# Optimization experiments

Measured on AMD Instinct MI355X. Metric: run time of the kernel, lower is better.

The kernel has to match this reference:

```python
import jax, jax.numpy as jnp
import numpy as np

N = 100000   # n_nodes
E = 1000000  # n_edges
B = 2000     # batch of interactions
K = 20       # n_neighbors
D = 172      # memory/node/edge/embedding dim
T = 172      # time encoding dim
MSG = 2 * D + D + T  # 688, identity message function
HEADS = 2


def setup_inputs() -> dict:
    key = jax.random.key(0)
    ks = jax.random.split(key, 32)
    g = lambda i, shape, fan: jax.random.normal(ks[i], shape, jnp.float32) / np.float32(np.sqrt(fan))
    inp = {}
    inp['memory'] = jax.random.normal(ks[0], (N, D), jnp.float32)
    inp['messages'] = jax.random.normal(ks[1], (N, MSG), jnp.float32)
    inp['edge_features'] = jax.random.normal(ks[2], (E, D), jnp.float32)
    inp['edge_times'] = jax.random.uniform(ks[3], (B,), jnp.float32) * 10000.0
    inp['neighbor_times'] = jax.random.uniform(ks[4], (3 * B, K), jnp.float32) * 10000.0
    # TimeEncode init: w = 1 / 10^linspace(0, 9, T)
    inp['time_w'] = jnp.asarray(1.0 / 10.0 ** np.linspace(0, 9, T), jnp.float32)
    inp['time_b'] = jnp.zeros((T,), jnp.float32)
    # GRUCell params
    inp['gru_w_ih'] = g(5, (3 * D, MSG), MSG)
    inp['gru_w_hh'] = g(6, (3 * D, D), D)
    inp['gru_b_ih'] = jnp.zeros((3 * D,), jnp.float32)
    inp['gru_b_hh'] = jnp.zeros((3 * D,), jnp.float32)
    # temporal attention params: query = [feat||time], key = [feat||edge||time]
    inp['w_q'] = g(7, (D, D + T), D + T)
    inp['w_k'] = g(8, (D, D + D + T), D + D + T)
    inp['w_v'] = g(9, (D, D + D + T), D + D + T)
    inp['w_o'] = g(10, (D, D), D)
    # MergeLayer(attn_out, src_feat)
    inp['merge_w1'] = g(11, (D, 2 * D), 2 * D)
    inp['merge_b1'] = jnp.zeros((D,), jnp.float32)
    inp['merge_w2'] = g(12, (D, D), D)
    inp['merge_b2'] = jnp.zeros((D,), jnp.float32)
    # affinity MergeLayer -> scalar score
    inp['aff_w1'] = g(13, (D, 2 * D), 2 * D)
    inp['aff_b1'] = jnp.zeros((D,), jnp.float32)
    inp['aff_w2'] = g(14, (1, D), D)
    inp['aff_b2'] = jnp.zeros((1,), jnp.float32)
    inp['source_nodes'] = jax.random.randint(ks[15], (B,), 0, N, jnp.int32)
    inp['destination_nodes'] = jax.random.randint(ks[16], (B,), 0, N, jnp.int32)
    inp['negative_nodes'] = jax.random.randint(ks[17], (B,), 0, N, jnp.int32)
    inp['neighbors'] = jax.random.randint(ks[18], (3 * B, K), 0, N, jnp.int32)
    inp['neighbor_edge_idxs'] = jax.random.randint(ks[19], (3 * B, K), 0, E, jnp.int32)
    return inp


def reference(memory, messages, edge_features, edge_times, neighbor_times,
              time_w, time_b, gru_w_ih, gru_w_hh, gru_b_ih, gru_b_hh,
              w_q, w_k, w_v, w_o, merge_w1, merge_b1, merge_w2, merge_b2,
              aff_w1, aff_b1, aff_w2, aff_b2,
              source_nodes, destination_nodes, negative_nodes,
              neighbors, neighbor_edge_idxs):
    d = memory.shape[1]
    dh = d // HEADS
    k_nbr = neighbors.shape[1]

    def time_enc(t):  # TimeEncode: cos(t * w + b)
        return jnp.cos(t[..., None] * time_w + time_b)

    # --- GRU memory update from aggregated ('last') messages ---
    gi = messages @ gru_w_ih.T + gru_b_ih          # [N, 3D]
    gh = memory @ gru_w_hh.T + gru_b_hh            # [N, 3D]
    i_r, i_z, i_n = jnp.split(gi, 3, axis=-1)
    h_r, h_z, h_n = jnp.split(gh, 3, axis=-1)
    r = jax.nn.sigmoid(i_r + h_r)
    z = jax.nn.sigmoid(i_z + h_z)
    n = jnp.tanh(i_n + r * h_n)
    mem_upd = (1.0 - z) * n + z * memory           # [N, D]

    # --- temporal graph attention embedding (1 layer) ---
    nodes = jnp.concatenate([source_nodes, destination_nodes, negative_nodes])  # [3B]
    ts = jnp.concatenate([edge_times, edge_times, edge_times])                  # [3B]
    m = nodes.shape[0]
    src_feat = mem_upd[nodes]                                                   # [3B, D]
    q_in = jnp.concatenate([src_feat, time_enc(jnp.zeros_like(ts))], axis=-1)   # [3B, D+T]
    nbr_feat = mem_upd[neighbors]                                               # [3B, K, D]
    e_feat = edge_features[neighbor_edge_idxs]                                  # [3B, K, D]
    dt = ts[:, None] - neighbor_times                                           # [3B, K]
    k_in = jnp.concatenate([nbr_feat, e_feat, time_enc(dt)], axis=-1)           # [3B, K, 2D+T]

    q = (q_in @ w_q.T).reshape(m, HEADS, dh)
    kk = (k_in @ w_k.T).reshape(m, k_nbr, HEADS, dh)
    vv = (k_in @ w_v.T).reshape(m, k_nbr, HEADS, dh)
    scores = jnp.einsum('nhd,nkhd->nhk', q, kk) / np.float32(np.sqrt(dh))
    valid = (neighbors > 0)[:, None, :]            # node 0 is the pad node
    scores = jnp.where(valid, scores, jnp.float32(-1e9))
    attn = jax.nn.softmax(scores, axis=-1)
    ctx = jnp.einsum('nhk,nkhd->nhd', attn, vv).reshape(m, d) @ w_o.T
    h1 = jax.nn.relu(jnp.concatenate([ctx, src_feat], axis=-1) @ merge_w1.T + merge_b1)
    emb = h1 @ merge_w2.T + merge_b2               # [3B, D]

    # --- affinity score on (src,dst) and (src,neg) pairs ---
    b = source_nodes.shape[0]
    s_emb, d_emb, n_emb = emb[:b], emb[b:2 * b], emb[2 * b:]
    s_cat = jnp.concatenate([s_emb, s_emb], axis=0)
    d_cat = jnp.concatenate([d_emb, n_emb], axis=0)
    ah = jax.nn.relu(jnp.concatenate([s_cat, d_cat], axis=-1) @ aff_w1.T + aff_b1)
    prob = jax.nn.sigmoid((ah @ aff_w2.T + aff_b2).squeeze(-1))  # [2B]
    return prob[:b], prob[b:]
```

## Files before the change

### kernel.cpp

```cpp
#include <hip/hip_runtime.h>
#include <math.h>

#define N_NODES 100000
#define BATCH   2000
#define KNBR    20
#define DF      172
#define MSGD    688
#define M3      6000
#define DH      86
#define KIN_D   516

#define KA      864
#define JP      768
#define KREAL   860
#define NTILES_N ((N_NODES + 127) / 128)
#define NWG_GRU (NTILES_N * 6)
#define KSTEPS  (KA / 32)

#define NKV     120000
#define KP_KV   544
#define JKV     384
#define KVS     352
#define NKV_TILES ((NKV + 127) / 128)

typedef __bf16 bf16x8 __attribute__((ext_vector_type(8)));
typedef __bf16 bf16x4 __attribute__((ext_vector_type(4)));
typedef float  f32x4  __attribute__((ext_vector_type(4)));

#define WPB_OFF   0
#define BP4_OFF   331776
#define WKV_OFF   332544
#define MU_OFF    436992
#define UNI_OFF   17636992
#define KV_OFF    UNI_OFF
#define QB_OFF    38756992
#define CAT_OFF   39286400
#define H1_OFF    40345216
#define EMBB_OFF  40922752
#define AH_OFF    41452160
#define MW1O_OFF  41812608
#define WQB_OFF   41842192
#define WM1B_OFF  41875984
#define WM2B_OFF  41909776
#define WAFFB_OFF 41928208
#define BM1P_OFF  41962000
#define BM2P_OFF  41962192
#define BAFFP_OFF 41962384
#define BQ0_OFF   41962576
#define NODES_OFF 41962768

__device__ __forceinline__ float sigmoidf_(float x) { return 1.0f / (1.0f + expf(-x)); }

typedef __attribute__((address_space(1))) const void gvoid;
typedef __attribute__((address_space(3))) void svoid;
__device__ __forceinline__ void gl16(const void* g, void* l) {
    __builtin_amdgcn_global_load_lds((gvoid*)g, (svoid*)l, 16, 0, 0);
}

__global__ __launch_bounds__(256) void prep_kernel(
    const float* __restrict__ w_ih, const float* __restrict__ w_hh,
    const float* __restrict__ b_ih, const float* __restrict__ b_hh,
    __bf16* __restrict__ wpb, float* __restrict__ bp4)
{
    int idx = blockIdx.x * 256 + threadIdx.x;
    if (idx < JP * KA) {
        int j = idx / KA, k = idx - j * KA;
        int d = j >> 2, g = j & 3;
        float v = 0.f;
        if (d < DF) {
            if (g == 0) {
                if (k < MSGD) v = w_ih[d * MSGD + k];
// ... 72 lines not shown
    const float* __restrict__ merge_w1, const float* __restrict__ w_o,
    float* __restrict__ mw1o)
{
    int idx = blockIdx.x * 256 + threadIdx.x;
    if (idx >= DF * DF) return;
    int j = idx / DF, k = idx - j * DF;
    float s = 0.f;
    for (int c = 0; c < DF; ++c)
        s = fmaf(merge_w1[j * 344 + c], w_o[c * DF + k], s);
    mw1o[idx] = s;
}

__global__ __launch_bounds__(256) void prep_tail_kernel(
    const float* __restrict__ w_q, const float* __restrict__ mw1o,
    const float* __restrict__ merge_w1, const float* __restrict__ merge_w2,
    const float* __restrict__ aff_w1,
    const float* __restrict__ merge_b1, const float* __restrict__ merge_b2,
    const float* __restrict__ aff_b1,
    const int* __restrict__ src_nodes, const int* __restrict__ dst_nodes,
    const int* __restrict__ neg_nodes,
    __bf16* __restrict__ wqb, __bf16* __restrict__ wm1b,
    __bf16* __restrict__ wm2b, __bf16* __restrict__ waffb,
    float* __restrict__ bm1p, float* __restrict__ bm2p,
    float* __restrict__ baffp, float* __restrict__ bq0,
    int* __restrict__ nodes_cat)
{
    int idx = blockIdx.x * 256 + threadIdx.x;
    if (idx < 192 * 352) {
        int j = idx / 352, k = idx - j * 352;
        float vq = 0.f, vm = 0.f, va = 0.f;
        if (j < DF) {
            if (k < DF) {
                vq = w_q[j * 344 + k];
                vm = mw1o[j * DF + k];
                va = aff_w1[j * 344 + k];
            } else if (k >= 176 && k < 348) {
                vq = w_q[j * 344 + 172 + (k - 176)];
                vm = merge_w1[j * 344 + 172 + (k - 176)];
                va = aff_w1[j * 344 + 172 + (k - 176)];
            }
        }
        wqb[idx] = (__bf16)vq;
        wm1b[idx] = (__bf16)vm;
        waffb[idx] = (__bf16)va;
    }
    if (idx < 192 * 192) {
        int j = idx / 192, k = idx - j * 192;
        wm2b[idx] = (__bf16)((j < DF && k < DF) ? merge_w2[j * DF + k] : 0.f);
    }
    if (idx < 192) {
        bm1p[idx]  = (idx < DF) ? merge_b1[idx] : 0.f;
        bm2p[idx]  = (idx < DF) ? merge_b2[idx] : 0.f;
        baffp[idx] = (idx < DF) ? aff_b1[idx] : 0.f;
        bq0[idx]   = 0.f;
    }
    if (idx < 6016) {
        int i = min(idx, M3 - 1);
        int node;
        if (i < BATCH)          node = src_nodes[i];
        else if (i < 2 * BATCH) node = dst_nodes[i - BATCH];
        else                    node = neg_nodes[i - 2 * BATCH];
        nodes_cat[idx] = node;
    }
}

__global__ __launch_bounds__(256) void gru_mfma3_kernel(
    const __bf16* __restrict__ xb, const __bf16* __restrict__ wpb,
    const float* __restrict__ bp4, const float* __restrict__ memory,
    float* __restrict__ mem_upd)
{
    __shared__ __align__(16) __bf16 Ws[3][128 * 32];
    __shared__ __align__(16) __bf16 Xs[3][128 * 32];

    const int t    = threadIdx.x;
    const int w    = t >> 6, lane = t & 63;
    const int lo   = lane & 15, hi = lane >> 4;
    const int wm   = w >> 1, wn = w & 1;

    const int orig = blockIdx.x;
    const int q = NWG_GRU >> 3, rr = NWG_GRU & 7;
    const int xcd = orig & 7, oidx = orig >> 3;
    const int wgid = (xcd < rr ? xcd * (q + 1) : rr * (q + 1) + (xcd - rr) * q) + oidx;
    const int m_tile = wgid % 6;
    const int n_tile = wgid / 6;
    const int n0 = n_tile * 128;
    const int j0 = m_tile * 128;

    const int srow  = lane >> 2;
    const int sslot = ((lane & 3) ^ ((lane >> 3) & 3)) * 8;

    f32x4 acc[4][4];
#pragma unroll
    for (int mi = 0; mi < 4; ++mi)
#pragma unroll
        for (int ni = 0; ni < 4; ++ni)
            acc[mi][ni] = (f32x4){0.f, 0.f, 0.f, 0.f};

    const __bf16* wbase = wpb + (size_t)j0 * KA;
    const __bf16* xbase = xb + (size_t)n0 * KA;

#define STAGE(buf, k0)                                                          \
    {                                                                           \
        _Pragma("unroll")                                                       \
        for (int qq = 0; qq < 2; ++qq) {                                        \
            const int lr = w * 32 + qq * 16 + srow;                             \
            gl16(wbase + (size_t)lr * KA + (k0) + sslot,                        \
                 &Ws[buf][(w * 32 + qq * 16) * 32]);                            \
            gl16(xbase + (size_t)lr * KA + (k0) + sslot,                        \
                 &Xs[buf][(w * 32 + qq * 16) * 32]);                            \
        }                                                                       \
    }

    STAGE(0, 0);
    STAGE(1, 32);

    const int fsa = (hi ^ ((lo >> 1) & 3)) * 8;
    for (int ks = 0; ks < KSTEPS; ++ks) {
        if (ks < KSTEPS - 1) {
            asm volatile("s_waitcnt vmcnt(4)" ::: "memory");
        } else {
            asm volatile("s_waitcnt vmcnt(0)" ::: "memory");
        }
        __builtin_amdgcn_s_barrier();
        if (ks + 2 < KSTEPS) STAGE((ks + 2) % 3, (ks + 2) * 32);

        const int bi = ks % 3;
        bf16x8 af[4], bx_[4];
#pragma unroll
        for (int i = 0; i < 4; ++i) {
            af[i]  = *(const bf16x8*)&Ws[bi][(wm * 64 + i * 16 + lo) * 32 + fsa];
            bx_[i] = *(const bf16x8*)&Xs[bi][(wn * 64 + i * 16 + lo) * 32 + fsa];
        }
#pragma unroll
        for (int mi = 0; mi < 4; ++mi)
#pragma unroll
            for (int ni = 0; ni < 4; ++ni)
                acc[mi][ni] = __builtin_amdgcn_mfma_f32_16x16x32_bf16(
                    af[mi], bx_[ni], acc[mi][ni], 0, 0, 0);
    }
#undef STAGE

    const int dbase = m_tile * 32 + wm * 16;
#pragma unroll
    for (int mi = 0; mi < 4; ++mi) {
        const int d = dbase + mi * 4 + hi;
        if (d >= DF) continue;
        const float4 b4 = *(const float4*)&bp4[4 * d];
#pragma unroll
        for (int ni = 0; ni < 4; ++ni) {
            const int n = n0 + wn * 64 + ni * 16 + lo;
            if (n >= N_NODES) continue;
            float sr  = acc[mi][ni][0] + b4.x;
            float sz  = acc[mi][ni][1] + b4.y;
            float gin = acc[mi][ni][2] + b4.z;
            float ghn = acc[mi][ni][3] + b4.w;
            float mem = memory[(size_t)n * DF + d];
            float rg  = sigmoidf_(sr);
            float zg  = sigmoidf_(sz);
            float nt  = tanhf(fmaf(rg, ghn, gin));
            mem_upd[(size_t)n * DF + d] = fmaf(zg, mem - nt, nt);
        }
    }
}

__global__ __launch_bounds__(256) void kv_gemm2_kernel(
    const float* __restrict__ mem_upd, const float* __restrict__ edge_features,
    const float* __restrict__ edge_times, const float* __restrict__ neighbor_times,
    const float* __restrict__ time_w, const float* __restrict__ time_b,
    const int* __restrict__ neighbors, const int* __restrict__ nbr_eidx,
    const __bf16* __restrict__ wkvb, __bf16* __restrict__ kv)
{
    __shared__ __align__(16) __bf16 Ws[128][32];
    __shared__ __align__(16) __bf16 Xs[128][32];

    const int t    = threadIdx.x;
    const int w    = t >> 6, lane = t & 63;
    const int lo   = lane & 15, hi = lane >> 4;
    const int wm   = w >> 1, wn = w & 1;

    const int bx     = blockIdx.x;
    const int n_tile = bx / 3;
    const int m_tile = bx - n_tile * 3;
    const int n0     = n_tile * 128;
    const int j0     = m_tile * 128;

    const int xrow  = t >> 1, xhalf = t & 1;
    const int nr    = min(n0 + xrow, NKV - 1);
    const int nbr   = neighbors[nr];
    const int eidx  = nbr_eidx[nr];
    const float dt  = edge_times[(nr / KNBR) % BATCH] - neighbor_times[nr];
    const float* mrow = mem_upd       + (size_t)nbr  * DF;
    const float* erow = edge_features + (size_t)eidx * DF;
    const __bf16* wrow = wkvb + (size_t)(j0 + xrow) * KP_KV;

    f32x4 acc[4][4];
#pragma unroll
    for (int mi = 0; mi < 4; ++mi)
#pragma unroll
        for (int ni = 0; ni < 4; ++ni)
            acc[mi][ni] = (f32x4){0.f, 0.f, 0.f, 0.f};

#define LOADX(k0, dst)                                                          \
    {                                                                           \
        _Pragma("unroll")                                                       \
        for (int c = 0; c < 4; ++c) {                                           \
            const int kb = (k0) + xhalf * 16 + c * 4;                           \
            float4 v;                                                           \
            if (kb < DF) {                                                      \
                v = *(const float4*)(mrow + kb);                                \
            } else if (kb < 2 * DF) {                                           \
                v = *(const float4*)(erow + (kb - DF));                         \
            } else if (kb < KIN_D) {                                            \
                const float4 tw = *(const float4*)(time_w + (kb - 2 * DF));     \
                const float4 tb = *(const float4*)(time_b + (kb - 2 * DF));     \
                v.x = cosf(fmaf(dt, tw.x, tb.x));                               \
                v.y = cosf(fmaf(dt, tw.y, tb.y));                               \
                v.z = cosf(fmaf(dt, tw.z, tb.z));                               \
                v.w = cosf(fmaf(dt, tw.w, tb.w));                               \
            } else {                                                            \
                v = make_float4(0.f, 0.f, 0.f, 0.f);                            \
            }                                                                   \
            dst[c] = v;                                                         \
        }                                                                       \
    }

    float4 xf[4];
    bf16x8 wp0, wp1;
    LOADX(0, xf);
    wp0 = *(const bf16x8*)(wrow + xhalf * 16);
    wp1 = *(const bf16x8*)(wrow + xhalf * 16 + 8);

    for (int ks = 0; ks < KP_KV / 32; ++ks) {
        const int k0 = ks * 32;
        bf16x8 x0, x1;
        x0[0]=(__bf16)xf[0].x; x0[1]=(__bf16)xf[0].y; x0[2]=(__bf16)xf[0].z; x0[3]=(__bf16)xf[0].w;
        x0[4]=(__bf16)xf[1].x; x0[5]=(__bf16)xf[1].y; x0[6]=(__bf16)xf[1].z; x0[7]=(__bf16)xf[1].w;
        x1[0]=(__bf16)xf[2].x; x1[1]=(__bf16)xf[2].y; x1[2]=(__bf16)xf[2].z; x1[3]=(__bf16)xf[2].w;
        x1[4]=(__bf16)xf[3].x; x1[5]=(__bf16)xf[3].y; x1[6]=(__bf16)xf[3].z; x1[7]=(__bf16)xf[3].w;
        *(bf16x8*)&Ws[xrow][xhalf * 16]     = wp0;
        *(bf16x8*)&Ws[xrow][xhalf * 16 + 8] = wp1;
        *(bf16x8*)&Xs[xrow][xhalf * 16]     = x0;
        *(bf16x8*)&Xs[xrow][xhalf * 16 + 8] = x1;

        if (ks + 1 < KP_KV / 32) {
            LOADX(k0 + 32, xf);
            wp0 = *(const bf16x8*)(wrow + k0 + 32 + xhalf * 16);
            wp1 = *(const bf16x8*)(wrow + k0 + 32 + xhalf * 16 + 8);
        }

        asm volatile("s_waitcnt lgkmcnt(0)" ::: "memory");
        __builtin_amdgcn_s_barrier();

        bf16x8 af[4], bx_[4];
#pragma unroll
        for (int i = 0; i < 4; ++i) {
            af[i]  = *(const bf16x8*)&Ws[wm * 64 + i * 16 + lo][hi * 8];
            bx_[i] = *(const bf16x8*)&Xs[wn * 64 + i * 16 + lo][hi * 8];
        }
#pragma unroll
        for (int mi = 0; mi < 4; ++mi)
#pragma unroll
            for (int ni = 0; ni < 4; ++ni)
                acc[mi][ni] = __builtin_amdgcn_mfma_f32_16x16x32_bf16(
                    af[mi], bx_[ni], acc[mi][ni], 0, 0, 0);

        __builtin_amdgcn_s_barrier();
    }
#undef LOADX

#pragma unroll
    for (int mi = 0; mi < 4; ++mi) {
        const int jb = j0 + wm * 64 + mi * 16 + hi * 4;
        int off;
        if (jb + 3 < DF)                 off = jb;
        else if (jb >= 192 && jb < 361)  off = jb - 16;
        else continue;
#pragma unroll
        for (int ni = 0; ni < 4; ++ni) {
            const int n = n0 + wn * 64 + ni * 16 + lo;
            if (n >= NKV) continue;
            bf16x4 o;
            o[0] = (__bf16)acc[mi][ni][0];
            o[1] = (__bf16)acc[mi][ni][1];
            o[2] = (__bf16)acc[mi][ni][2];
            o[3] = (__bf16)acc[mi][ni][3];
            *(bf16x4*)(kv + (size_t)n * KVS + off) = o;
        }
    }
}

template<int MODE, int KP>
__global__ __launch_bounds__(256) void tail_gemm_kernel(
    const __bf16* __restrict__ wb, const float* __restrict__ bias,
    const void* __restrict__ actsrc, const float* __restrict__ time_b,
    const int* __restrict__ nodes_cat,
    __bf16* __restrict__ outb, int ostride, int jmax, int nrows, int relu)
{
    __shared__ __align__(16) __bf16 Ws[128][32];
    __shared__ __align__(16) __bf16 Xs[128][32];

    const int t    = threadIdx.x;
    const int w    = t >> 6, lane = t & 63;
    const int lo   = lane & 15, hi = lane >> 4;
    const int wm   = w >> 1, wn = w & 1;

    const int n_tile = blockIdx.x >> 1;
    const int j0     = (blockIdx.x & 1) * 64;
    const int n0     = n_tile * 128;

    const int xrow  = t >> 1, xhalf = t & 1;
    const int nr    = min(n0 + xrow, nrows - 1);
    const __bf16* wrow = wb + (size_t)(j0 + xrow) * KP;

    f32x4 acc[4][4];
#pragma unroll
    for (int mi = 0; mi < 4; ++mi)
#pragma unroll
        for (int ni = 0; ni < 4; ++ni)
            acc[mi][ni] = (f32x4){0.f, 0.f, 0.f, 0.f};

    for (int k0 = 0; k0 < KP; k0 += 32) {
        bf16x8 w0 = *(const bf16x8*)(wrow + k0 + xhalf * 16);
        bf16x8 w1 = *(const bf16x8*)(wrow + k0 + xhalf * 16 + 8);
        bf16x8 x0, x1;
        const int kb16 = k0 + xhalf * 16;
        if constexpr (MODE == 0) {
            const float* mrow = (const float*)actsrc + (size_t)nodes_cat[nr] * DF;
            float fl[16];
#pragma unroll
            for (int c = 0; c < 4; ++c) {
                const int b = kb16 + c * 4;
                float4 v;
                if (b + 3 < DF) v = *(const float4*)(mrow + b);
                else if (b >= 176 && b < 348) {
                    const float4 tb = *(const float4*)(time_b + (b - 176));
                    v.x = cosf(tb.x); v.y = cosf(tb.y);
                    v.z = cosf(tb.z); v.w = cosf(tb.w);
                } else v = make_float4(0.f, 0.f, 0.f, 0.f);
                fl[c*4+0]=v.x; fl[c*4+1]=v.y; fl[c*4+2]=v.z; fl[c*4+3]=v.w;
            }
#pragma unroll
            for (int jj = 0; jj < 8; ++jj) { x0[jj]=(__bf16)fl[jj]; x1[jj]=(__bf16)fl[8+jj]; }
        } else if constexpr (MODE == 1) {
            const __bf16* arow = (const __bf16*)actsrc + (size_t)nr * KP;
            x0 = *(const bf16x8*)(arow + kb16);
            x1 = *(const bf16x8*)(arow + kb16 + 8);
        } else {
            const int s = (nr < BATCH) ? nr : nr - BATCH;
            const __bf16* eb = (const __bf16*)actsrc;
            const __bf16* src = (kb16 < 176) ? (eb + (size_t)s * 176 + kb16)
                                             : (eb + (size_t)(nr + BATCH) * 176 + (kb16 - 176));
            x0 = *(const bf16x8*)src;
            x1 = *(const bf16x8*)(src + 8);
        }
        *(bf16x8*)&Ws[xrow][xhalf * 16]     = w0;
        *(bf16x8*)&Ws[xrow][xhalf * 16 + 8] = w1;
        *(bf16x8*)&Xs[xrow][xhalf * 16]     = x0;
        *(bf16x8*)&Xs[xrow][xhalf * 16 + 8] = x1;
        __syncthreads();

        bf16x8 af[4], bx_[4];
#pragma unroll
        for (int i = 0; i < 4; ++i) {
            af[i]  = *(const bf16x8*)&Ws[wm * 64 + i * 16 + lo][hi * 8];
            bx_[i] = *(const bf16x8*)&Xs[wn * 64 + i * 16 + lo][hi * 8];
        }
#pragma unroll
        for (int mi = 0; mi < 4; ++mi)
#pragma unroll
            for (int ni = 0; ni < 4; ++ni)
                acc[mi][ni] = __builtin_amdgcn_mfma_f32_16x16x32_bf16(
                    af[mi], bx_[ni], acc[mi][ni], 0, 0, 0);
        __syncthreads();
    }

#pragma unroll
    for (int mi = 0; mi < 4; ++mi) {
        const int jb = j0 + wm * 64 + mi * 16 + hi * 4;
        if (jb + 3 >= jmax) continue;
        const float4 b4 = *(const float4*)(bias + jb);
#pragma unroll
        for (int ni = 0; ni < 4; ++ni) {
            const int n = n0 + wn * 64 + ni * 16 + lo;
            if (n >= nrows) continue;
            float v0 = acc[mi][ni][0] + b4.x;
            float v1 = acc[mi][ni][1] + b4.y;
            float v2 = acc[mi][ni][2] + b4.z;
            float v3 = acc[mi][ni][3] + b4.w;
            if (relu) {
                v0 = fmaxf(v0, 0.f); v1 = fmaxf(v1, 0.f);
                v2 = fmaxf(v2, 0.f); v3 = fmaxf(v3, 0.f);
            }
            bf16x4 o;
            o[0]=(__bf16)v0; o[1]=(__bf16)v1; o[2]=(__bf16)v2; o[3]=(__bf16)v3;
            *(bf16x4*)(outb + (size_t)n * ostride + jb) = o;
        }
    }
}

__global__ __launch_bounds__(256) void attn_mid_kernel(
    const float* __restrict__ mem_upd, const __bf16* __restrict__ kv,
    const __bf16* __restrict__ qb, const int* __restrict__ neighbors,
    const int* __restrict__ nodes_cat, __bf16* __restrict__ cat)
{
    __shared__ __align__(16) __bf16 kvs[KNBR][KVS];
    __shared__ float qs[176];
    __shared__ float scl[2][KNBR];
    __shared__ float attnl[2][KNBR];
    __shared__ int   nbrs[KNBR];

    const int i = blockIdx.x;
    const int t = threadIdx.x;

    if (t < KNBR) nbrs[t] = neighbors[i * KNBR + t];
    if (t < 176) qs[t] = (float)qb[(size_t)i * 176 + t];
    {
        const uint4* src = (const uint4*)(kv + (size_t)i * KNBR * KVS);
        uint4* dst = (uint4*)&kvs[0][0];
        for (int idx = t; idx < KNBR * KVS / 8; idx += 256) dst[idx] = src[idx];
    }
    __syncthreads();

    if (t < 2 * KNBR) {
        int h = t / KNBR, kn = t - h * KNBR;
// ... 1 lines not shown
#pragma unroll 2
        for (int j = 0; j < DH; ++j)
            s = fmaf(qs[h * DH + j], (float)kvs[kn][h * DH + j], s);
        s /= sqrtf((float)DH);
        scl[h][kn] = (nbrs[kn] > 0) ? s : -1e9f;
    }
    __syncthreads();
    if (t < 2) {
        float m = -INFINITY;
        for (int kn = 0; kn < KNBR; ++kn) m = fmaxf(m, scl[t][kn]);
        float se = 0.f;
        for (int kn = 0; kn < KNBR; ++kn) se += expf(scl[t][kn] - m);
        float inv = 1.f / se;
        for (int kn = 0; kn < KNBR; ++kn) attnl[t][kn] = expf(scl[t][kn] - m) * inv;
    }
    __syncthreads();
    if (t < DF) {
        int h = t / DH;
        float cx = 0.f;
#pragma unroll
        for (int kn = 0; kn < KNBR; ++kn)
            cx = fmaf(attnl[h][kn], (float)kvs[kn][176 + t], cx);
        cat[(size_t)i * 352 + t] = (__bf16)cx;
        cat[(size_t)i * 352 + 176 + t] =
            (__bf16)mem_upd[(size_t)nodes_cat[i] * DF + t];
    }
    if (t < 4) {
        cat[(size_t)i * 352 + 172 + t] = (__bf16)0.f;
        cat[(size_t)i * 352 + 348 + t] = (__bf16)0.f;
    }
}

__global__ __launch_bounds__(256) void aff_fin_kernel(
    const __bf16* __restrict__ ah, const float* __restrict__ aff_w2,
    const float* __restrict__ aff_b2, float* __restrict__ out)
{
    const int t = threadIdx.x;
    const int w = t >> 6, lane = t & 63;
    const int row = blockIdx.x * 4 + w;
    if (row >= 2 * BATCH) return;
    float s = 0.f;
    if (lane < DF)       s += (float)ah[(size_t)row * 176 + lane] * aff_w2[lane];
    if (lane + 64 < DF)  s += (float)ah[(size_t)row * 176 + lane + 64] * aff_w2[lane + 64];
    if (lane + 128 < DF) s += (float)ah[(size_t)row * 176 + lane + 128] * aff_w2[lane + 128];
#pragma unroll
    for (int off = 32; off > 0; off >>= 1) s += __shfl_down(s, off, 64);
    if (lane == 0) out[row] = 1.f / (1.f + expf(-(s + aff_b2[0])));
}

extern "C" void kernel_launch(void* const* d_in, const int* in_sizes, int n_in,
                              void* d_out, int out_size, void* d_ws, size_t ws_size,
                              hipStream_t stream)
{
    (void)in_sizes; (void)n_in; (void)out_size; (void)ws_size;
    const float* memory         = (const float*)d_in[0];
    const float* messages       = (const float*)d_in[1];
    const float* edge_features  = (const float*)d_in[2];
    const float* edge_times     = (const float*)d_in[3];
    const float* neighbor_times = (const float*)d_in[4];
    const float* time_w         = (const float*)d_in[5];
    const float* time_b         = (const float*)d_in[6];
    const float* gru_w_ih       = (const float*)d_in[7];
    const float* gru_w_hh       = (const float*)d_in[8];
    const float* gru_b_ih       = (const float*)d_in[9];
    const float* gru_b_hh       = (const float*)d_in[10];
    const float* w_q            = (const float*)d_in[11];
    const float* w_k            = (const float*)d_in[12];
    const float* w_v            = (const float*)d_in[13];
    const float* w_o            = (const float*)d_in[14];
    const float* merge_w1       = (const float*)d_in[15];
    const float* merge_b1       = (const float*)d_in[16];
    const float* merge_w2       = (const float*)d_in[17];
    const float* merge_b2       = (const float*)d_in[18];
    const float* aff_w1         = (const float*)d_in[19];
    const float* aff_b1         = (const float*)d_in[20];
    const float* aff_w2         = (const float*)d_in[21];
    const float* aff_b2         = (const float*)d_in[22];
    const int* src_nodes        = (const int*)d_in[23];
    const int* dst_nodes        = (const int*)d_in[24];
    const int* neg_nodes        = (const int*)d_in[25];
    const int* neighbors        = (const int*)d_in[26];
    const int* nbr_eidx         = (const int*)d_in[27];

    float* ws       = (float*)d_ws;
    __bf16* wpb     = (__bf16*)(ws + WPB_OFF);
    float* bp4      = ws + BP4_OFF;
    __bf16* wkvb    = (__bf16*)(ws + WKV_OFF);
    float* mem_upd  = ws + MU_OFF;
    __bf16* xbuf    = (__bf16*)(ws + UNI_OFF);
    __bf16* kv      = (__bf16*)(ws + KV_OFF);
    __bf16* qbuf    = (__bf16*)(ws + QB_OFF);
    __bf16* cat     = (__bf16*)(ws + CAT_OFF);
    __bf16* h1      = (__bf16*)(ws + H1_OFF);
    __bf16* embb    = (__bf16*)(ws + EMBB_OFF);
    __bf16* ah      = (__bf16*)(ws + AH_OFF);
    float* mw1o     = ws + MW1O_OFF;
    __bf16* wqb     = (__bf16*)(ws + WQB_OFF);
    __bf16* wm1b    = (__bf16*)(ws + WM1B_OFF);
    __bf16* wm2b    = (__bf16*)(ws + WM2B_OFF);
    __bf16* waffb   = (__bf16*)(ws + WAFFB_OFF);
    float* bm1p     = ws + BM1P_OFF;
    float* bm2p     = ws + BM2P_OFF;
    float* baffp    = ws + BAFFP_OFF;
    float* bq0      = ws + BQ0_OFF;
    int*   nodes_cat= (int*)(ws + NODES_OFF);
    float* out      = (float*)d_out;

    prep_kernel<<<(JP * KA + 255) / 256, 256, 0, stream>>>(
        gru_w_ih, gru_w_hh, gru_b_ih, gru_b_hh, wpb, bp4);
    prep_kv_kernel<<<(JKV * KP_KV + 255) / 256, 256, 0, stream>>>(w_k, w_v, wkvb);
    conv_kernel<<<2048, 256, 0, stream>>>(messages, memory, xbuf);
    gru_mfma3_kernel<<<NWG_GRU, 256, 0, stream>>>(xbuf, wpb, bp4, memory, mem_upd);
    mw1o_kernel<<<(DF * DF + 255) / 256, 256, 0, stream>>>(merge_w1, w_o, mw1o);
    prep_tail_kernel<<<(192 * 352 + 255) / 256, 256, 0, stream>>>(
        w_q, mw1o, merge_w1, merge_w2, aff_w1, merge_b1, merge_b2, aff_b1,
        src_nodes, dst_nodes, neg_nodes,
        wqb, wm1b, wm2b, waffb, bm1p, bm2p, baffp, bq0, nodes_cat);
    kv_gemm2_kernel<<<NKV_TILES * 3, 256, 0, stream>>>(
        mem_upd, edge_features, edge_times, neighbor_times, time_w, time_b,
        neighbors, nbr_eidx, wkvb, kv);
    tail_gemm_kernel<0, 352><<<47 * 2, 256, 0, stream>>>(
        wqb, bq0, mem_upd, time_b, nodes_cat, qbuf, 176, 176, M3, 0);
    attn_mid_kernel<<<M3, 256, 0, stream>>>(
        mem_upd, kv, qbuf, neighbors, nodes_cat, cat);
    tail_gemm_kernel<1, 352><<<47 * 2, 256, 0, stream>>>(
        wm1b, bm1p, cat, nullptr, nullptr, h1, 192, 192, M3, 1);
    tail_gemm_kernel<1, 192><<<47 * 2, 256, 0, stream>>>(
        wm2b, bm2p, h1, nullptr, nullptr, embb, 176, 176, M3, 0);
    tail_gemm_kernel<2, 352><<<32 * 2, 256, 0, stream>>>(
        waffb, baffp, embb, nullptr, nullptr, ah, 176, 176, 2 * BATCH, 1);
    aff_fin_kernel<<<(2 * BATCH + 3) / 4, 256, 0, stream>>>(ah, aff_w2, aff_b2, out);
}
```

Measured before the change: 763.5 us.

## Widen GRU tiles, store memory in bf16, fuse merge and affinity tail GEMMs

The GRU GEMM now computes 128x256 tiles per workgroup, doubling the node dimension, so each staged weight tile is reused over more nodes. The updated memory is stored as bf16 rather than fp32, which halves its write traffic and the gather reads in the KV, Q and attention kernels. The two merge-layer GEMMs become one kernel with h1 kept in shared memory, and the affinity GEMM is fused with the final dot-product and sigmoid, dropping several launches and intermediate buffers. The risks are extra rounding on memory values and higher register and LDS use in the wider GRU kernel, which may lower occupancy.

```diff
diff --git a/kernel.cpp b/kernel.cpp
--- a/kernel.cpp
+++ b/kernel.cpp
@@ -13,9 +13,9 @@
 #define KA      864
 #define JP      768
 #define KREAL   860
-#define NTILES_N ((N_NODES + 127) / 128)
-#define NWG_GRU (NTILES_N * 6)
 #define KSTEPS  (KA / 32)
+#define NTILES4 391
+#define NWG4    (NTILES4 * 6)
 
 #define NKV     120000
 #define KP_KV   544
@@ -35,9 +35,7 @@
 #define KV_OFF    UNI_OFF
 #define QB_OFF    38756992
 #define CAT_OFF   39286400
-#define H1_OFF    40345216
 #define EMBB_OFF  40922752
-#define AH_OFF    41452160
 #define MW1O_OFF  41812608
 #define WQB_OFF   41842192
 #define WM1B_OFF  41875984
@@ -46,7 +44,6 @@
 #define BM1P_OFF  41962000
 #define BM2P_OFF  41962192
 #define BAFFP_OFF 41962384
-#define BQ0_OFF   41962576
 #define NODES_OFF 41962768
 
 __device__ __forceinline__ float sigmoidf_(float x) { return 1.0f / (1.0f + expf(-x)); }
@@ -165,8 +162,7 @@
     __bf16* __restrict__ wqb, __bf16* __restrict__ wm1b,
     __bf16* __restrict__ wm2b, __bf16* __restrict__ waffb,
     float* __restrict__ bm1p, float* __restrict__ bm2p,
-    float* __restrict__ baffp, float* __restrict__ bq0,
-    int* __restrict__ nodes_cat)
+    float* __restrict__ baffp, int* __restrict__ nodes_cat)
 {
     int idx = blockIdx.x * 256 + threadIdx.x;
     if (idx < 192 * 352) {
@@ -195,7 +191,6 @@
         bm1p[idx]  = (idx < DF) ? merge_b1[idx] : 0.f;
         bm2p[idx]  = (idx < DF) ? merge_b2[idx] : 0.f;
         baffp[idx] = (idx < DF) ? aff_b1[idx] : 0.f;
-        bq0[idx]   = 0.f;
     }
     if (idx < 6016) {
         int i = min(idx, M3 - 1);
@@ -207,13 +202,13 @@
     }
 }
 
-__global__ __launch_bounds__(256) void gru_mfma3_kernel(
+__global__ __launch_bounds__(256) void gru_mfma4_kernel(
     const __bf16* __restrict__ xb, const __bf16* __restrict__ wpb,
     const float* __restrict__ bp4, const float* __restrict__ memory,
-    float* __restrict__ mem_upd)
+    __bf16* __restrict__ mem_upd)
 {
     __shared__ __align__(16) __bf16 Ws[3][128 * 32];
-    __shared__ __align__(16) __bf16 Xs[3][128 * 32];
+    __shared__ __align__(16) __bf16 Xs[3][256 * 32];
 
     const int t    = threadIdx.x;
     const int w    = t >> 6, lane = t & 63;
@@ -221,22 +216,22 @@
     const int wm   = w >> 1, wn = w & 1;
 
     const int orig = blockIdx.x;
-    const int q = NWG_GRU >> 3, rr = NWG_GRU & 7;
+    const int q = NWG4 >> 3, rr = NWG4 & 7;
     const int xcd = orig & 7, oidx = orig >> 3;
     const int wgid = (xcd < rr ? xcd * (q + 1) : rr * (q + 1) + (xcd - rr) * q) + oidx;
     const int m_tile = wgid % 6;
     const int n_tile = wgid / 6;
-    const int n0 = n_tile * 128;
+    const int n0 = n_tile * 256;
     const int j0 = m_tile * 128;
 
     const int srow  = lane >> 2;
     const int sslot = ((lane & 3) ^ ((lane >> 3) & 3)) * 8;
 
-    f32x4 acc[4][4];
+    f32x4 acc[4][8];
 #pragma unroll
     for (int mi = 0; mi < 4; ++mi)
 #pragma unroll
-        for (int ni = 0; ni < 4; ++ni)
+        for (int ni = 0; ni < 8; ++ni)
             acc[mi][ni] = (f32x4){0.f, 0.f, 0.f, 0.f};
 
     const __bf16* wbase = wpb + (size_t)j0 * KA;
@@ -249,8 +244,12 @@
             const int lr = w * 32 + qq * 16 + srow;                             \
             gl16(wbase + (size_t)lr * KA + (k0) + sslot,                        \
                  &Ws[buf][(w * 32 + qq * 16) * 32]);                            \
+        }                                                                       \
+        _Pragma("unroll")                                                       \
+        for (int qq = 0; qq < 4; ++qq) {                                        \
+            const int lr = w * 64 + qq * 16 + srow;                             \
             gl16(xbase + (size_t)lr * KA + (k0) + sslot,                        \
-                 &Xs[buf][(w * 32 + qq * 16) * 32]);                            \
+                 &Xs[buf][(w * 64 + qq * 16) * 32]);                            \
         }                                                                       \
     }
 
@@ -260,7 +259,7 @@
     const int fsa = (hi ^ ((lo >> 1) & 3)) * 8;
     for (int ks = 0; ks < KSTEPS; ++ks) {
         if (ks < KSTEPS - 1) {
-            asm volatile("s_waitcnt vmcnt(4)" ::: "memory");
+            asm volatile("s_waitcnt vmcnt(6)" ::: "memory");
         } else {
             asm volatile("s_waitcnt vmcnt(0)" ::: "memory");
         }
@@ -268,18 +267,19 @@
         if (ks + 2 < KSTEPS) STAGE((ks + 2) % 3, (ks + 2) * 32);
 
         const int bi = ks % 3;
-        bf16x8 af[4], bx_[4];
-#pragma unroll
-        for (int i = 0; i < 4; ++i) {
+        bf16x8 af[4], bxv[8];
+#pragma unroll
+        for (int i = 0; i < 4; ++i)
             af[i]  = *(const bf16x8*)&Ws[bi][(wm * 64 + i * 16 + lo) * 32 + fsa];
-            bx_[i] = *(const bf16x8*)&Xs[bi][(wn * 64 + i * 16 + lo) * 32 + fsa];
-        }
+#pragma unroll
+        for (int i = 0; i < 8; ++i)
+            bxv[i] = *(const bf16x8*)&Xs[bi][(wn * 128 + i * 16 + lo) * 32 + fsa];
 #pragma unroll
         for (int mi = 0; mi < 4; ++mi)
 #pragma unroll
-            for (int ni = 0; ni < 4; ++ni)
+            for (int ni = 0; ni < 8; ++ni)
                 acc[mi][ni] = __builtin_amdgcn_mfma_f32_16x16x32_bf16(
-                    af[mi], bx_[ni], acc[mi][ni], 0, 0, 0);
+                    af[mi], bxv[ni], acc[mi][ni], 0, 0, 0);
     }
 #undef STAGE
 
@@ -290,8 +290,8 @@
         if (d >= DF) continue;
         const float4 b4 = *(const float4*)&bp4[4 * d];
 #pragma unroll
-        for (int ni = 0; ni < 4; ++ni) {
-            const int n = n0 + wn * 64 + ni * 16 + lo;
+        for (int ni = 0; ni < 8; ++ni) {
+            const int n = n0 + wn * 128 + ni * 16 + lo;
             if (n >= N_NODES) continue;
             float sr  = acc[mi][ni][0] + b4.x;
             float sz  = acc[mi][ni][1] + b4.y;
@@ -301,13 +301,13 @@
             float rg  = sigmoidf_(sr);
             float zg  = sigmoidf_(sz);
             float nt  = tanhf(fmaf(rg, ghn, gin));
-            mem_upd[(size_t)n * DF + d] = fmaf(zg, mem - nt, nt);
-        }
-    }
-}
-
-__global__ __launch_bounds__(256) void kv_gemm2_kernel(
-    const float* __restrict__ mem_upd, const float* __restrict__ edge_features,
+            mem_upd[(size_t)n * DF + d] = (__bf16)fmaf(zg, mem - nt, nt);
+        }
+    }
+}
+
+__global__ __launch_bounds__(256) void kv_gemm3_kernel(
+    const __bf16* __restrict__ mem_upd, const float* __restrict__ edge_features,
     const float* __restrict__ edge_times, const float* __restrict__ neighbor_times,
     const float* __restrict__ time_w, const float* __restrict__ time_b,
     const int* __restrict__ neighbors, const int* __restrict__ nbr_eidx,
@@ -332,8 +332,8 @@
     const int nbr   = neighbors[nr];
     const int eidx  = nbr_eidx[nr];
     const float dt  = edge_times[(nr / KNBR) % BATCH] - neighbor_times[nr];
-    const float* mrow = mem_upd       + (size_t)nbr  * DF;
-    const float* erow = edge_features + (size_t)eidx * DF;
+    const __bf16* mrow = mem_upd       + (size_t)nbr  * DF;
+    const float*  erow = edge_features + (size_t)eidx * DF;
     const __bf16* wrow = wkvb + (size_t)(j0 + xrow) * KP_KV;
 
     f32x4 acc[4][4];
@@ -343,50 +343,60 @@
         for (int ni = 0; ni < 4; ++ni)
             acc[mi][ni] = (f32x4){0.f, 0.f, 0.f, 0.f};
 
-#define LOADX(k0, dst)                                                          \
+#define LOADX(k0, xh, xf)                                                       \
     {                                                                           \
         _Pragma("unroll")                                                       \
         for (int c = 0; c < 4; ++c) {                                           \
             const int kb = (k0) + xhalf * 16 + c * 4;                           \
-            float4 v;                                                           \
             if (kb < DF) {                                                      \
-                v = *(const float4*)(mrow + kb);                                \
+                xh[c] = *(const bf16x4*)(mrow + kb);                            \
             } else if (kb < 2 * DF) {                                           \
-                v = *(const float4*)(erow + (kb - DF));                         \
+                xf[c] = *(const float4*)(erow + (kb - DF));                     \
             } else if (kb < KIN_D) {                                            \
                 const float4 tw = *(const float4*)(time_w + (kb - 2 * DF));     \
                 const float4 tb = *(const float4*)(time_b + (kb - 2 * DF));     \
+                float4 v;                                                       \
                 v.x = cosf(fmaf(dt, tw.x, tb.x));                               \
                 v.y = cosf(fmaf(dt, tw.y, tb.y));                               \
                 v.z = cosf(fmaf(dt, tw.z, tb.z));                               \
                 v.w = cosf(fmaf(dt, tw.w, tb.w));                               \
+                xf[c] = v;                                                      \
             } else {                                                            \
-                v = make_float4(0.f, 0.f, 0.f, 0.f);                            \
+                xf[c] = make_float4(0.f, 0.f, 0.f, 0.f);                        \
             }                                                                   \
-            dst[c] = v;                                                         \
         }                                                                       \
     }
 
+    bf16x4 xh[4];
     float4 xf[4];
     bf16x8 wp0, wp1;
-    LOADX(0, xf);
+    LOADX(0, xh, xf);
     wp0 = *(const bf16x8*)(wrow + xhalf * 16);
     wp1 = *(const bf16x8*)(wrow + xhalf * 16 + 8);
 
     for (int ks = 0; ks < KP_KV / 32; ++ks) {
         const int k0 = ks * 32;
         bf16x8 x0, x1;
-        x0[0]=(__bf16)xf[0].x; x0[1]=(__bf16)xf[0].y; x0[2]=(__bf16)xf[0].z; x0[3]=(__bf16)xf[0].w;
-        x0[4]=(__bf16)xf[1].x; x0[5]=(__bf16)xf[1].y; x0[6]=(__bf16)xf[1].z; x0[7]=(__bf16)xf[1].w;
-        x1[0]=(__bf16)xf[2].x; x1[1]=(__bf16)xf[2].y; x1[2]=(__bf16)xf[2].z; x1[3]=(__bf16)xf[2].w;
-        x1[4]=(__bf16)xf[3].x; x1[5]=(__bf16)xf[3].y; x1[6]=(__bf16)xf[3].z; x1[7]=(__bf16)xf[3].w;
+#pragma unroll
+        for (int c = 0; c < 4; ++c) {
+            const int kb = k0 + xhalf * 16 + c * 4;
+            __bf16 e0, e1, e2, e3;
+            if (kb < DF) {
+                e0 = xh[c][0]; e1 = xh[c][1]; e2 = xh[c][2]; e3 = xh[c][3];
+            } else {
+                e0 = (__bf16)xf[c].x; e1 = (__bf16)xf[c].y;
+                e2 = (__bf16)xf[c].z; e3 = (__bf16)xf[c].w;
+            }
+            if (c < 2) { x0[c*4]=e0; x0[c*4+1]=e1; x0[c*4+2]=e2; x0[c*4+3]=e3; }
+            else { x1[(c-2)*4]=e0; x1[(c-2)*4+1]=e1; x1[(c-2)*4+2]=e2; x1[(c-2)*4+3]=e3; }
+        }
         *(bf16x8*)&Ws[xrow][xhalf * 16]     = wp0;
         *(bf16x8*)&Ws[xrow][xhalf * 16 + 8] = wp1;
         *(bf16x8*)&Xs[xrow][xhalf * 16]     = x0;
         *(bf16x8*)&Xs[xrow][xhalf * 16 + 8] = x1;
 
         if (ks + 1 < KP_KV / 32) {
-            LOADX(k0 + 32, xf);
+            LOADX(k0 + 32, xh, xf);
             wp0 = *(const bf16x8*)(wrow + k0 + 32 + xhalf * 16);
             wp1 = *(const bf16x8*)(wrow + k0 + 32 + xhalf * 16 + 8);
         }
@@ -432,12 +442,10 @@
     }
 }
 
-template<int MODE, int KP>
-__global__ __launch_bounds__(256) void tail_gemm_kernel(
-    const __bf16* __restrict__ wb, const float* __restrict__ bias,
-    const void* __restrict__ actsrc, const float* __restrict__ time_b,
-    const int* __restrict__ nodes_cat,
-    __bf16* __restrict__ outb, int ostride, int jmax, int nrows, int relu)
+__global__ __launch_bounds__(256) void q_gemm_kernel(
+    const __bf16* __restrict__ wqb, const __bf16* __restrict__ mem_upd,
+    const float* __restrict__ time_b, const int* __restrict__ nodes_cat,
+    __bf16* __restrict__ qbuf)
 {
     __shared__ __align__(16) __bf16 Ws[128][32];
     __shared__ __align__(16) __bf16 Xs[128][32];
@@ -452,8 +460,9 @@
     const int n0     = n_tile * 128;
 
     const int xrow  = t >> 1, xhalf = t & 1;
-    const int nr    = min(n0 + xrow, nrows - 1);
-    const __bf16* wrow = wb + (size_t)(j0 + xrow) * KP;
+    const int nr    = min(n0 + xrow, M3 - 1);
+    const __bf16* mrow = mem_upd + (size_t)nodes_cat[nr] * DF;
+    const __bf16* wrow = wqb + (size_t)(j0 + xrow) * 352;
 
     f32x4 acc[4][4];
 #pragma unroll
@@ -462,39 +471,26 @@
         for (int ni = 0; ni < 4; ++ni)
             acc[mi][ni] = (f32x4){0.f, 0.f, 0.f, 0.f};
 
-    for (int k0 = 0; k0 < KP; k0 += 32) {
+    for (int k0 = 0; k0 < 352; k0 += 32) {
         bf16x8 w0 = *(const bf16x8*)(wrow + k0 + xhalf * 16);
         bf16x8 w1 = *(const bf16x8*)(wrow + k0 + xhalf * 16 + 8);
         bf16x8 x0, x1;
-        const int kb16 = k0 + xhalf * 16;
-        if constexpr (MODE == 0) {
-            const float* mrow = (const float*)actsrc + (size_t)nodes_cat[nr] * DF;
-            float fl[16];
-#pragma unroll
-            for (int c = 0; c < 4; ++c) {
-                const int b = kb16 + c * 4;
-                float4 v;
-                if (b + 3 < DF) v = *(const float4*)(mrow + b);
-                else if (b >= 176 && b < 348) {
-                    const float4 tb = *(const float4*)(time_b + (b - 176));
-                    v.x = cosf(tb.x); v.y = cosf(tb.y);
-                    v.z = cosf(tb.z); v.w = cosf(tb.w);
-                } else v = make_float4(0.f, 0.f, 0.f, 0.f);
-                fl[c*4+0]=v.x; fl[c*4+1]=v.y; fl[c*4+2]=v.z; fl[c*4+3]=v.w;
+#pragma unroll
+        for (int c = 0; c < 4; ++c) {
+            const int b = k0 + xhalf * 16 + c * 4;
+            __bf16 e0, e1, e2, e3;
+            if (b + 3 < DF) {
+                bf16x4 h = *(const bf16x4*)(mrow + b);
+                e0 = h[0]; e1 = h[1]; e2 = h[2]; e3 = h[3];
+            } else if (b >= 176 && b < 348) {
+                const float4 tb = *(const float4*)(time_b + (b - 176));
+                e0 = (__bf16)cosf(tb.x); e1 = (__bf16)cosf(tb.y);
+                e2 = (__bf16)cosf(tb.z); e3 = (__bf16)cosf(tb.w);
+            } else {
+                e0 = e1 = e2 = e3 = (__bf16)0.f;
             }
-#pragma unroll
-            for (int jj = 0; jj < 8; ++jj) { x0[jj]=(__bf16)fl[jj]; x1[jj]=(__bf16)fl[8+jj]; }
-        } else if constexpr (MODE == 1) {
-            const __bf16* arow = (const __bf16*)actsrc + (size_t)nr * KP;
-            x0 = *(const bf16x8*)(arow + kb16);
-            x1 = *(const bf16x8*)(arow + kb16 + 8);
-        } else {
-            const int s = (nr < BATCH) ? nr : nr - BATCH;
-            const __bf16* eb = (const __bf16*)actsrc;
-            const __bf16* src = (kb16 < 176) ? (eb + (size_t)s * 176 + kb16)
-                                             : (eb + (size_t)(nr + BATCH) * 176 + (kb16 - 176));
-            x0 = *(const bf16x8*)src;
-            x1 = *(const bf16x8*)(src + 8);
+            if (c < 2) { x0[c*4]=e0; x0[c*4+1]=e1; x0[c*4+2]=e2; x0[c*4+3]=e3; }
+            else { x1[(c-2)*4]=e0; x1[(c-2)*4+1]=e1; x1[(c-2)*4+2]=e2; x1[(c-2)*4+3]=e3; }
         }
         *(bf16x8*)&Ws[xrow][xhalf * 16]     = w0;
         *(bf16x8*)&Ws[xrow][xhalf * 16 + 8] = w1;
@@ -520,29 +516,21 @@
 #pragma unroll
     for (int mi = 0; mi < 4; ++mi) {
         const int jb = j0 + wm * 64 + mi * 16 + hi * 4;
-        if (jb + 3 >= jmax) continue;
-        const float4 b4 = *(const float4*)(bias + jb);
+        if (jb + 3 >= 176) continue;
 #pragma unroll
         for (int ni = 0; ni < 4; ++ni) {
             const int n = n0 + wn * 64 + ni * 16 + lo;
-            if (n >= nrows) continue;
-            float v0 = acc[mi][ni][0] + b4.x;
-            float v1 = acc[mi][ni][1] + b4.y;
-            float v2 = acc[mi][ni][2] + b4.z;
-            float v3 = acc[mi][ni][3] + b4.w;
-            if (relu) {
-                v0 = fmaxf(v0, 0.f); v1 = fmaxf(v1, 0.f);
-                v2 = fmaxf(v2, 0.f); v3 = fmaxf(v3, 0.f);
-            }
+            if (n >= M3) continue;
             bf16x4 o;
-            o[0]=(__bf16)v0; o[1]=(__bf16)v1; o[2]=(__bf16)v2; o[3]=(__bf16)v3;
-            *(bf16x4*)(outb + (size_t)n * ostride + jb) = o;
+            o[0]=(__bf16)acc[mi][ni][0]; o[1]=(__bf16)acc[mi][ni][1];
+            o[2]=(__bf16)acc[mi][ni][2]; o[3]=(__bf16)acc[mi][ni][3];
+            *(bf16x4*)(qbuf + (size_t)n * 176 + jb) = o;
         }
     }
 }
 
 __global__ __launch_bounds__(256) void attn_mid_kernel(
-    const float* __restrict__ mem_upd, const __bf16* __restrict__ kv,
+    const __bf16* __restrict__ mem_upd, const __bf16* __restrict__ kv,
     const __bf16* __restrict__ qb, const int* __restrict__ neighbors,
     const int* __restrict__ nodes_cat, __bf16* __restrict__ cat)
 {
@@ -590,8 +578,7 @@
         for (int kn = 0; kn < KNBR; ++kn)
             cx = fmaf(attnl[h][kn], (float)kvs[kn][176 + t], cx);
         cat[(size_t)i * 352 + t] = (__bf16)cx;
-        cat[(size_t)i * 352 + 176 + t] =
-            (__bf16)mem_upd[(size_t)nodes_cat[i] * DF + t];
+        cat[(size_t)i * 352 + 176 + t] = mem_upd[(size_t)nodes_cat[i] * DF + t];
     }
     if (t < 4) {
         cat[(size_t)i * 352 + 172 + t] = (__bf16)0.f;
@@ -599,21 +586,225 @@
     }
 }
 
-__global__ __launch_bounds__(256) void aff_fin_kernel(
-    const __bf16* __restrict__ ah, const float* __restrict__ aff_w2,
+__global__ __launch_bounds__(256) void merge_emb_kernel(
+    const __bf16* __restrict__ cat, const __bf16* __restrict__ wm1b,
+    const __bf16* __restrict__ wm2b, const float* __restrict__ bm1p,
+    const float* __restrict__ bm2p, __bf16* __restrict__ embb)
+{
+    __shared__ __align__(16) __bf16 Ws[192 * 32];
+    __shared__ __align__(16) __bf16 Xs[128 * 32];
+    __shared__ __align__(16) __bf16 h1[128 * 200];
+
+    const int t    = threadIdx.x;
+    const int w    = t >> 6, lane = t & 63;
+    const int lo   = lane & 15, hi = lane >> 4;
+    const int wm   = w >> 1, wn = w & 1;
+    const int n0   = blockIdx.x * 128;
+
+    const int srow  = lane >> 2;
+    const int sslot = ((lane & 3) ^ ((lane >> 3) & 3)) * 8;
+    const int fsa   = (hi ^ ((lo >> 1) & 3)) * 8;
+
+    f32x4 acc[6][4];
+#pragma unroll
+    for (int mi = 0; mi < 6; ++mi)
+#pragma unroll
+        for (int ni = 0; ni < 4; ++ni)
+            acc[mi][ni] = (f32x4){0.f, 0.f, 0.f, 0.f};
+
+    for (int k0 = 0; k0 < 352; k0 += 32) {
+#pragma unroll
+        for (int qq = 0; qq < 3; ++qq) {
+            const int jr = w * 48 + qq * 16 + srow;
+            gl16(wm1b + (size_t)jr * 352 + k0 + sslot, &Ws[(w * 48 + qq * 16) * 32]);
+        }
+#pragma unroll
+        for (int qq = 0; qq < 2; ++qq) {
+            const int r = w * 32 + qq * 16 + srow;
+            const int nr = min(n0 + r, M3 - 1);
+            gl16(cat + (size_t)nr * 352 + k0 + sslot, &Xs[(w * 32 + qq * 16) * 32]);
+        }
+        asm volatile("s_waitcnt vmcnt(0)" ::: "memory");
+        __syncthreads();
+
+        bf16x8 af[6], bx_[4];
+#pragma unroll
+        for (int i = 0; i < 6; ++i)
+            af[i] = *(const bf16x8*)&Ws[(wm * 96 + i * 16 + lo) * 32 + fsa];
+#pragma unroll
+        for (int i = 0; i < 4; ++i)
+            bx_[i] = *(const bf16x8*)&Xs[(wn * 64 + i * 16 + lo) * 32 + fsa];
+#pragma unroll
+        for (int mi = 0; mi < 6; ++mi)
+#pragma unroll
+            for (int ni = 0; ni < 4; ++ni)
+                acc[mi][ni] = __builtin_amdgcn_mfma_f32_16x16x32_bf16(
+                    af[mi], bx_[ni], acc[mi][ni], 0, 0, 0);
+        __syncthreads();
+    }
+
+#pragma unroll
+    for (int mi = 0; mi < 6; ++mi) {
+        const int jb = wm * 96 + mi * 16 + hi * 4;
+        const float4 b4 = *(const float4*)(bm1p + jb);
+#pragma unroll
+        for (int ni = 0; ni < 4; ++ni) {
+            const int nl = wn * 64 + ni * 16 + lo;
+            bf16x4 o;
+            o[0] = (__bf16)fmaxf(acc[mi][ni][0] + b4.x, 0.f);
+            o[1] = (__bf16)fmaxf(acc[mi][ni][1] + b4.y, 0.f);
+            o[2] = (__bf16)fmaxf(acc[mi][ni][2] + b4.z, 0.f);
+            o[3] = (__bf16)fmaxf(acc[mi][ni][3] + b4.w, 0.f);
+            *(bf16x4*)&h1[nl * 200 + jb] = o;
+        }
+    }
+    __syncthreads();
+
+    f32x4 acc2[6][4];
+#pragma unroll
+    for (int mi = 0; mi < 6; ++mi)
+#pragma unroll
+        for (int ni = 0; ni < 4; ++ni)
+            acc2[mi][ni] = (f32x4){0.f, 0.f, 0.f, 0.f};
+
+    for (int k0 = 0; k0 < 192; k0 += 32) {
+#pragma unroll
+        for (int qq = 0; qq < 3; ++qq) {
+            const int jr = w * 48 + qq * 16 + srow;
+            gl16(wm2b + (size_t)jr * 192 + k0 + sslot, &Ws[(w * 48 + qq * 16) * 32]);
+        }
+        asm volatile("s_waitcnt vmcnt(0)" ::: "memory");
+        __syncthreads();
+
+        bf16x8 af[6], bx_[4];
+#pragma unroll
+        for (int i = 0; i < 6; ++i)
+            af[i] = *(const bf16x8*)&Ws[(wm * 96 + i * 16 + lo) * 32 + fsa];
+#pragma unroll
+        for (int i = 0; i < 4; ++i)
+            bx_[i] = *(const bf16x8*)&h1[(wn * 64 + i * 16 + lo) * 200 + k0 + hi * 8];
+#pragma unroll
+        for (int mi = 0; mi < 6; ++mi)
+#pragma unroll
+            for (int ni = 0; ni < 4; ++ni)
+                acc2[mi][ni] = __builtin_amdgcn_mfma_f32_16x16x32_bf16(
+                    af[mi], bx_[ni], acc2[mi][ni], 0, 0, 0);
+        __syncthreads();
+    }
+
+#pragma unroll
+    for (int mi = 0; mi < 6; ++mi) {
+        const int jb = wm * 96 + mi * 16 + hi * 4;
+        if (jb + 3 >= 176) continue;
+        const float4 b4 = *(const float4*)(bm2p + jb);
+#pragma unroll
+        for (int ni = 0; ni < 4; ++ni) {
+            const int n = n0 + wn * 64 + ni * 16 + lo;
+            if (n >= M3) continue;
+            bf16x4 o;
+            o[0] = (__bf16)(acc2[mi][ni][0] + b4.x);
+            o[1] = (__bf16)(acc2[mi][ni][1] + b4.y);
+            o[2] = (__bf16)(acc2[mi][ni][2] + b4.z);
+            o[3] = (__bf16)(acc2[mi][ni][3] + b4.w);
+            *(bf16x4*)(embb + (size_t)n * 176 + jb) = o;
+        }
+    }
+}
+
+__global__ __launch_bounds__(256) void aff_fused_kernel(
+    const __bf16* __restrict__ embb, const __bf16* __restrict__ waffb,
+    const float* __restrict__ baffp, const float* __restrict__ aff_w2,
     const float* __restrict__ aff_b2, float* __restrict__ out)
 {
-    const int t = threadIdx.x;
-    const int w = t >> 6, lane = t & 63;
-    const int row = blockIdx.x * 4 + w;
-    if (row >= 2 * BATCH) return;
-    float s = 0.f;
-    if (lane < DF)       s += (float)ah[(size_t)row * 176 + lane] * aff_w2[lane];
-    if (lane + 64 < DF)  s += (float)ah[(size_t)row * 176 + lane + 64] * aff_w2[lane + 64];
-    if (lane + 128 < DF) s += (float)ah[(size_t)row * 176 + lane + 128] * aff_w2[lane + 128];
-#pragma unroll
-    for (int off = 32; off > 0; off >>= 1) s += __shfl_down(s, off, 64);
-    if (lane == 0) out[row] = 1.f / (1.f + expf(-(s + aff_b2[0])));
+    __shared__ __align__(16) __bf16 Ws[192 * 32];
+    __shared__ __align__(16) __bf16 Xs[128 * 32];
+    __shared__ float sred[2][2][4][16];
+
+    const int t    = threadIdx.x;
+    const int w    = t >> 6, lane = t & 63;
+    const int lo   = lane & 15, hi = lane >> 4;
+    const int wm   = w >> 1, wn = w & 1;
+    const int n0   = blockIdx.x * 128;
+
+    const int srow  = lane >> 2;
+    const int sslot = ((lane & 3) ^ ((lane >> 3) & 3)) * 8;
+    const int fsa   = (hi ^ ((lo >> 1) & 3)) * 8;
+
+    f32x4 acc[6][4];
+#pragma unroll
+    for (int mi = 0; mi < 6; ++mi)
+#pragma unroll
+        for (int ni = 0; ni < 4; ++ni)
+            acc[mi][ni] = (f32x4){0.f, 0.f, 0.f, 0.f};
+
+    for (int k0 = 0; k0 < 352; k0 += 32) {
+#pragma unroll
+        for (int qq = 0; qq < 3; ++qq) {
+            const int jr = w * 48 + qq * 16 + srow;
+            gl16(waffb + (size_t)jr * 352 + k0 + sslot, &Ws[(w * 48 + qq * 16) * 32]);
+        }
+#pragma unroll
+        for (int qq = 0; qq < 2; ++qq) {
+            const int r = w * 32 + qq * 16 + srow;
+            const int nr = min(n0 + r, 2 * BATCH - 1);
+            const int s  = (nr < BATCH) ? nr : nr - BATCH;
+            const int col = k0 + sslot;
+            const __bf16* src = (col < 176)
+                ? embb + (size_t)s * 176 + col
+                : embb + (size_t)(nr + BATCH) * 176 + (col - 176);
+            gl16(src, &Xs[(w * 32 + qq * 16) * 32]);
+        }
+        asm volatile("s_waitcnt vmcnt(0)" ::: "memory");
+        __syncthreads();
+
+        bf16x8 af[6], bx_[4];
+#pragma unroll
+        for (int i = 0; i < 6; ++i)
+            af[i] = *(const bf16x8*)&Ws[(wm * 96 + i * 16 + lo) * 32 + fsa];
+#pragma unroll
+        for (int i = 0; i < 4; ++i)
+            bx_[i] = *(const bf16x8*)&Xs[(wn * 64 + i * 16 + lo) * 32 + fsa];
+#pragma unroll
+        for (int mi = 0; mi < 6; ++mi)
+#pragma unroll
+            for (int ni = 0; ni < 4; ++ni)
+                acc[mi][ni] = __builtin_amdgcn_mfma_f32_16x16x32_bf16(
+                    af[mi], bx_[ni], acc[mi][ni], 0, 0, 0);
+        __syncthreads();
+    }
+
+    float ps[4] = {0.f, 0.f, 0.f, 0.f};
+#pragma unroll
+    for (int mi = 0; mi < 6; ++mi) {
+        const int jb = wm * 96 + mi * 16 + hi * 4;
+#pragma unroll
+        for (int r = 0; r < 4; ++r) {
+            const int j = jb + r;
+            const float w2v = (j < DF) ? aff_w2[j] : 0.f;
+            const float bb  = baffp[j];
+#pragma unroll
+            for (int ni = 0; ni < 4; ++ni)
+                ps[ni] += fmaxf(acc[mi][ni][r] + bb, 0.f) * w2v;
+        }
+    }
+#pragma unroll
+    for (int ni = 0; ni < 4; ++ni) {
+        ps[ni] += __shfl_xor(ps[ni], 16, 64);
+        ps[ni] += __shfl_xor(ps[ni], 32, 64);
+    }
+    if (hi == 0) {
+#pragma unroll
+        for (int ni = 0; ni < 4; ++ni) sred[wm][wn][ni][lo] = ps[ni];
+    }
+    __syncthreads();
+    if (t < 128) {
+        const int n = n0 + t;
+        if (n < 2 * BATCH) {
+            const int wn2 = t >> 6, ni = (t >> 4) & 3, lo2 = t & 15;
+            float s = sred[0][wn2][ni][lo2] + sred[1][wn2][ni][lo2] + aff_b2[0];
+            out[n] = 1.f / (1.f + expf(-s));
+        }
+    }
 }
 
 extern "C" void kernel_launch(void* const* d_in, const int* in_sizes, int n_in,
@@ -654,14 +845,12 @@
     __bf16* wpb     = (__bf16*)(ws + WPB_OFF);
     float* bp4      = ws + BP4_OFF;
     __bf16* wkvb    = (__bf16*)(ws + WKV_OFF);
-    float* mem_upd  = ws + MU_OFF;
+    __bf16* mem_upd = (__bf16*)(ws + MU_OFF);
     __bf16* xbuf    = (__bf16*)(ws + UNI_OFF);
     __bf16* kv      = (__bf16*)(ws + KV_OFF);
     __bf16* qbuf    = (__bf16*)(ws + QB_OFF);
     __bf16* cat     = (__bf16*)(ws + CAT_OFF);
-    __bf16* h1      = (__bf16*)(ws + H1_OFF);
     __bf16* embb    = (__bf16*)(ws + EMBB_OFF);
-    __bf16* ah      = (__bf16*)(ws + AH_OFF);
     float* mw1o     = ws + MW1O_OFF;
     __bf16* wqb     = (__bf16*)(ws + WQB_OFF);
     __bf16* wm1b    = (__bf16*)(ws + WM1B_OFF);
@@ -670,7 +859,6 @@
     float* bm1p     = ws + BM1P_OFF;
     float* bm2p     = ws + BM2P_OFF;
     float* baffp    = ws + BAFFP_OFF;
-    float* bq0      = ws + BQ0_OFF;
     int*   nodes_cat= (int*)(ws + NODES_OFF);
     float* out      = (float*)d_out;
 
@@ -678,24 +866,18 @@
         gru_w_ih, gru_w_hh, gru_b_ih, gru_b_hh, wpb, bp4);
     prep_kv_kernel<<<(JKV * KP_KV + 255) / 256, 256, 0, stream>>>(w_k, w_v, wkvb);
     conv_kernel<<<2048, 256, 0, stream>>>(messages, memory, xbuf);
-    gru_mfma3_kernel<<<NWG_GRU, 256, 0, stream>>>(xbuf, wpb, bp4, memory, mem_upd);
+    gru_mfma4_kernel<<<NWG4, 256, 0, stream>>>(xbuf, wpb, bp4, memory, mem_upd);
     mw1o_kernel<<<(DF * DF + 255) / 256, 256, 0, stream>>>(merge_w1, w_o, mw1o);
     prep_tail_kernel<<<(192 * 352 + 255) / 256, 256, 0, stream>>>(
         w_q, mw1o, merge_w1, merge_w2, aff_w1, merge_b1, merge_b2, aff_b1,
         src_nodes, dst_nodes, neg_nodes,
-        wqb, wm1b, wm2b, waffb, bm1p, bm2p, baffp, bq0, nodes_cat);
-    kv_gemm2_kernel<<<NKV_TILES * 3, 256, 0, stream>>>(
+        wqb, wm1b, wm2b, waffb, bm1p, bm2p, baffp, nodes_cat);
+    kv_gemm3_kernel<<<NKV_TILES * 3, 256, 0, stream>>>(
         mem_upd, edge_features, edge_times, neighbor_times, time_w, time_b,
         neighbors, nbr_eidx, wkvb, kv);
-    tail_gemm_kernel<0, 352><<<47 * 2, 256, 0, stream>>>(
-        wqb, bq0, mem_upd, time_b, nodes_cat, qbuf, 176, 176, M3, 0);
+    q_gemm_kernel<<<47 * 2, 256, 0, stream>>>(wqb, mem_upd, time_b, nodes_cat, qbuf);
     attn_mid_kernel<<<M3, 256, 0, stream>>>(
         mem_upd, kv, qbuf, neighbors, nodes_cat, cat);
-    tail_gemm_kernel<1, 352><<<47 * 2, 256, 0, stream>>>(
-        wm1b, bm1p, cat, nullptr, nullptr, h1, 192, 192, M3, 1);
-    tail_gemm_kernel<1, 192><<<47 * 2, 256, 0, stream>>>(
-        wm2b, bm2p, h1, nullptr, nullptr, embb, 176, 176, M3, 0);
-    tail_gemm_kernel<2, 352><<<32 * 2, 256, 0, stream>>>(
-        waffb, baffp, embb, nullptr, nullptr, ah, 176, 176, 2 * BATCH, 1);
-    aff_fin_kernel<<<(2 * BATCH + 3) / 4, 256, 0, stream>>>(ah, aff_w2, aff_b2, out);
-}
+    merge_emb_kernel<<<47, 256, 0, stream>>>(cat, wm1b, wm2b, bm1p, bm2p, embb);
+    aff_fused_kernel<<<32, 256, 0, stream>>>(embb, waffb, baffp, aff_w2, aff_b2, out);
+}
```

After: 986.1 us. 29.2% more time.
